# Optimization experiments

Measured on AMD Instinct MI355X. Metric: run time of the kernel, lower is better.

Reference implementation:

```python
import jax, jax.numpy as jnp
import numpy as np

EPS = 1e-5

def conv1x1(x, w, b):
    # x: [B,C,H,W], w: [O,C], b: [O]
    return jnp.einsum('bchw,oc->bohw', x, w) + b[None, :, None, None]

def bn(x, gamma, beta, mean, var):
    scale = gamma / jnp.sqrt(var + EPS)
    return x * scale[None, :, None, None] + (beta - mean * scale)[None, :, None, None]

def setup_inputs() -> dict:
    B, C, H, W = 8, 256, 64, 64
    F0, F1 = 128, 128
    key = jax.random.key(0)
    ks = jax.random.split(key, 16)
    d = {}
    d['inputs'] = jax.random.normal(ks[0], (B, C, H, W), dtype=jnp.float32)
    def make_cna(i, fout, fin):
        w = jax.random.normal(ks[i], (fout, fin), dtype=jnp.float32) / np.sqrt(fin)
        b = jnp.zeros((fout,), dtype=jnp.float32)
        g = jnp.ones((fout,), dtype=jnp.float32)
        be = jnp.zeros((fout,), dtype=jnp.float32)
        m = 0.1 * jax.random.normal(ks[i + 1], (fout,), dtype=jnp.float32)
        v = jax.random.uniform(ks[i + 2], (fout,), dtype=jnp.float32, minval=0.5, maxval=1.5)
        return w, b, g, be, m, v
    (d['theta_w'], d['theta_b'], d['theta_g'], d['theta_beta'], d['theta_m'], d['theta_v']) = make_cna(1, F0, C)
    (d['phi_w'], d['phi_b'], d['phi_g'], d['phi_beta'], d['phi_m'], d['phi_v']) = make_cna(4, F0, C)
    (d['mu_w'], d['mu_b'], d['mu_g'], d['mu_beta'], d['mu_m'], d['mu_v']) = make_cna(7, F1, C)
    d['pre_w'] = jax.random.normal(ks[10], (C, F1), dtype=jnp.float32) / np.sqrt(F1)
    d['pre_b'] = jnp.zeros((C,), dtype=jnp.float32)
    d['post_g'] = jnp.ones((C,), dtype=jnp.float32)
    d['post_beta'] = jnp.zeros((C,), dtype=jnp.float32)
    d['post_m'] = 0.1 * jax.random.normal(ks[11], (C,), dtype=jnp.float32)
    d['post_v'] = jax.random.uniform(ks[12], (C,), dtype=jnp.float32, minval=0.5, maxval=1.5)
    return d

def reference(inputs, theta_w, theta_b, theta_g, theta_beta, theta_m, theta_v,
              phi_w, phi_b, phi_g, phi_beta, phi_m, phi_v,
              mu_w, mu_b, mu_g, mu_beta, mu_m, mu_v,
              pre_w, pre_b, post_g, post_beta, post_m, post_v):
    B, C, H, W = inputs.shape
    N = H * W
    # theta/phi/mu: 1x1 conv + batchnorm (eval) + relu
    t = jax.nn.relu(bn(conv1x1(inputs, theta_w, theta_b), theta_g, theta_beta, theta_m, theta_v))
    p = jax.nn.relu(bn(conv1x1(inputs, phi_w, phi_b), phi_g, phi_beta, phi_m, phi_v))
    z = jax.nn.relu(bn(conv1x1(inputs, mu_w, mu_b), mu_g, mu_beta, mu_m, mu_v))
    tf = t.reshape(B, -1, N)   # [B,F0,N]
    pf = p.reshape(B, -1, N)   # [B,F0,N]
    zf = z.reshape(B, -1, N)   # [B,F1,N]
    # unscaled softmax(theta^T phi) mu^T, batched (original loops over B)
    attn = jax.nn.softmax(jnp.einsum('bfn,bfm->bnm', tf, pf), axis=-1)  # [B,N,N]
    u = jnp.einsum('bnm,bfm->bfn', attn, zf).reshape(B, -1, H, W)       # [B,F1,H,W]
    pre = conv1x1(u, pre_w, pre_b)                                       # [B,C,H,W]
    return jax.nn.relu(bn(pre + inputs, post_g, post_beta, post_m, post_v))
```

## Files before the change

### kernel.cpp

```cpp
#include <hip/hip_runtime.h>

typedef __attribute__((ext_vector_type(8))) _Float16 f16x8;
typedef __attribute__((ext_vector_type(4))) float f32x4;
typedef __attribute__((ext_vector_type(16))) float f32x16;
typedef __attribute__((ext_vector_type(4))) unsigned u32x4;

#define EPSV 1e-5f
#define BB 8
#define CC 256
#define NP 4096
#define FF 128
#define SPLIT 4
#define CHUNK 1024
#define NIT 16

#define GLD16(gp, lp) __builtin_amdgcn_global_load_lds( \
    (const __attribute__((address_space(1))) unsigned int*)(gp), \
    (__attribute__((address_space(3))) unsigned int*)(lp), 16, 0, 0)

static __device__ __forceinline__ unsigned short f2h(float f) {
    union { _Float16 h; unsigned short u; } v;
    v.h = (_Float16)f;
    return v.u;
}
static __device__ __forceinline__ float h2f(unsigned short u) {
    union { unsigned short u; _Float16 h; } v;
    v.u = u;
    return (float)v.h;
}

struct PrepArgs {
    const float* w[3]; const float* bias[3]; const float* g[3]; const float* be[3];
    const float* m[3]; const float* v[3];
    const float* pre_w; const float* pre_b;
    const float* post_g; const float* post_be; const float* post_m; const float* post_v;
    unsigned short* W_all; float* b_all; unsigned short* W2; float* b2; float* sres;
};

__global__ __launch_bounds__(256) void prep_kernel(PrepArgs a) {
    int idx = blockIdx.x * 256 + threadIdx.x;
    if (idx < 3 * 128 * 256) {
        int row = idx >> 8, c = idx & 255;
        int which = row >> 7, f = row & 127;
        float s = a.g[which][f] * rsqrtf(a.v[which][f] + EPSV);
        a.W_all[idx] = f2h(a.w[which][f * 256 + c] * s);
        if (c == 0)
            a.b_all[row] = s * a.bias[which][f] + a.be[which][f] - a.m[which][f] * s;
    } else {
        int i = idx - 3 * 128 * 256;
        if (i < 256 * 128) {
            int c = i >> 7, f = i & 127;
            float s = a.post_g[c] * rsqrtf(a.post_v[c] + EPSV);
            a.W2[i] = f2h(a.pre_w[i] * s);
            if (f == 0) {
                a.b2[c] = s * a.pre_b[c] + a.post_be[c] - a.post_m[c] * s;
                a.sres[c] = s;
            }
        }
    }
}

__global__ __launch_bounds__(256) void transpose_x_kernel(const float* __restrict__ x,
                                                          unsigned short* __restrict__ xT) {
    __shared__ float tile[64][65];
    int blk = blockIdx.x;
    int b  = blk >> 8;
    int c0 = ((blk >> 6) & 3) << 6;
    int n0 = (blk & 63) << 6;
    int t = threadIdx.x;
    const float* src = x + ((size_t)b * CC + c0) * NP + n0;
    #pragma unroll
    for (int i = 0; i < 16; ++i) {
        int cl = i * 4 + (t >> 6);
        tile[cl][t & 63] = src[(size_t)cl * NP + (t & 63)];
    }
    __syncthreads();
    unsigned short* dst = xT + ((size_t)b * NP + n0) * CC + c0;
    #pragma unroll
    for (int i = 0; i < 8; ++i) {
        int nl = i * 8 + (t >> 5);
        int cl = (t & 31) * 2;
        unsigned lo = f2h(tile[cl][nl]);
        unsigned hi = f2h(tile[cl + 1][nl]);
        *reinterpret_cast<unsigned*>(dst + (size_t)nl * CC + cl) = (hi << 16) | lo;
    }
}

__global__ __launch_bounds__(256) void qkv_kernel(const unsigned short* __restrict__ xT,
                                                  const unsigned short* __restrict__ W_all,
                                                  const float* __restrict__ b_all,
                                                  unsigned short* __restrict__ tq,
                                                  unsigned short* __restrict__ kp,
                                                  unsigned short* __restrict__ vz) {
    __shared__ unsigned short Alds[128 * 72];
    __shared__ unsigned short Blds[128 * 72];
    int blk = blockIdx.x;
    int b  = blk & 7;
    int r  = blk >> 3;
    int ft = r >> 5;
    int n0 = (r & 31) << 7;
    int fbase = ft << 7;
    int t = threadIdx.x, w = t >> 6, l = t & 63;
    int wr = (w >> 1) << 6, wc = (w & 1) << 6;
    const unsigned short* A  = xT + ((size_t)b * NP + n0) * CC;
    const unsigned short* Bw = W_all + (size_t)fbase * CC;

    f32x4 acc[4][4];
    #pragma unroll
    for (int i = 0; i < 4; ++i)
        #pragma unroll
        for (int j = 0; j < 4; ++j)
            acc[i][j] = f32x4{0.f, 0.f, 0.f, 0.f};

    for (int c0 = 0; c0 < 256; c0 += 64) {
        #pragma unroll
        for (int i = 0; i < 4; ++i) {
            int row = i * 32 + (t >> 3);
            int ch = (t & 7) * 8;
            *reinterpret_cast<int4*>(&Alds[row * 72 + ch]) =
                *reinterpret_cast<const int4*>(A + (size_t)row * CC + c0 + ch);
            *reinterpret_cast<int4*>(&Blds[row * 72 + ch]) =
                *reinterpret_cast<const int4*>(Bw + (size_t)row * CC + c0 + ch);
        }
        __syncthreads();
        #pragma unroll
        for (int kk = 0; kk < 2; ++kk) {
            f16x8 af[4], bfr[4];
            #pragma unroll
            for (int mi = 0; mi < 4; ++mi)
                af[mi] = *reinterpret_cast<const f16x8*>(
                    &Alds[(wr + mi * 16 + (l & 15)) * 72 + kk * 32 + (l >> 4) * 8]);
            #pragma unroll
            for (int ni = 0; ni < 4; ++ni)
                bfr[ni] = *reinterpret_cast<const f16x8*>(
                    &Blds[(wc + ni * 16 + (l & 15)) * 72 + kk * 32 + (l >> 4) * 8]);
            #pragma unroll
            for (int mi = 0; mi < 4; ++mi)
                #pragma unroll
                for (int ni = 0; ni < 4; ++ni)
                    acc[mi][ni] = __builtin_amdgcn_mfma_f32_16x16x32_f16(af[mi], bfr[ni], acc[mi][ni], 0, 0, 0);
        }
        __syncthreads();
    }

    #pragma unroll
    for (int mi = 0; mi < 4; ++mi) {
        #pragma unroll
        for (int ni = 0; ni < 4; ++ni) {
            int fl = wc + ni * 16 + (l & 15);
            float bias = b_all[fbase + fl];
            int nb = n0 + wr + mi * 16 + ((l >> 4) << 2);
            if (ft == 2) {
                unsigned pk0, pk1;
                float v0 = acc[mi][ni][0] + bias; v0 = v0 > 0.f ? v0 : 0.f;
                float v1 = acc[mi][ni][1] + bias; v1 = v1 > 0.f ? v1 : 0.f;
                float v2 = acc[mi][ni][2] + bias; v2 = v2 > 0.f ? v2 : 0.f;
                float v3 = acc[mi][ni][3] + bias; v3 = v3 > 0.f ? v3 : 0.f;
                pk0 = (unsigned)f2h(v0) | ((unsigned)f2h(v1) << 16);
                pk1 = (unsigned)f2h(v2) | ((unsigned)f2h(v3) << 16);
                uint2 uu; uu.x = pk0; uu.y = pk1;
                *reinterpret_cast<uint2*>(vz + (size_t)b * FF * NP + (size_t)fl * NP + nb) = uu;
            } else {
                unsigned short* dst = (ft == 0 ? tq : kp) + (size_t)b * NP * FF;
                #pragma unroll
                for (int rg = 0; rg < 4; ++rg) {
                    float v = acc[mi][ni][rg] + bias;
                    dst[(size_t)(nb + rg) * FF + fl] = f2h(v > 0.f ? v : 0.f);
                }
            }
        }
    }
}

__global__ __launch_bounds__(256, 2) void attn_kernel(const unsigned short* __restrict__ tq,
                                                      const unsigned short* __restrict__ kp,
                                                      const unsigned short* __restrict__ vz,
                                                      unsigned short* __restrict__ Uh,
                                                      float2* __restrict__ ml) {
    __shared__ unsigned short Kl[2][8192];
    __shared__ unsigned short Vl[2][8192];
    int blk = blockIdx.x;
    int b = blk & 7;
    int rest = blk >> 3;
    int s = rest & 3;
    int qt = rest >> 2;
    int t = threadIdx.x, w = t >> 6, l = t & 63;
    int r = l & 31, h = l >> 5, lx = l & 7;
    int n0w = qt * 128 + w * 32;
    int mbase = s * CHUNK;
    const unsigned short* Q = tq + (size_t)b * NP * FF;
    const unsigned short* K = kp + (size_t)b * NP * FF;
    const unsigned short* V = vz + (size_t)b * FF * NP;

    f16x8 qf[8];
    #pragma unroll
    for (int kf = 0; kf < 8; ++kf)
        qf[kf] = *reinterpret_cast<const f16x8*>(Q + (size_t)(n0w + r) * FF + kf * 16 + h * 8);

    f32x16 U[4];
    #pragma unroll
    for (int fb = 0; fb < 4; ++fb)
        #pragma unroll
        for (int i = 0; i < 16; ++i) U[fb][i] = 0.f;
    float mrun = -1e30f, lrun = 0.f;

    const unsigned short* kbase[4];
    const unsigned short* vbase[4];
    #pragma unroll
    for (int i = 0; i < 4; ++i) {
        int seg = w * 4 + i;
        int krow = seg * 4 + (l >> 4);
        kbase[i] = K + (size_t)(mbase + krow) * FF + 8 * ((l & 15) ^ (krow & 7));
        int frow = seg * 8 + (l >> 3);
        vbase[i] = V + (size_t)frow * NP + mbase + 8 * ((l & 7) ^ (frow & 7));
    }

    #pragma unroll
    for (int i = 0; i < 4; ++i) {
        GLD16(kbase[i], &Kl[0][(w * 4 + i) * 512]);
        GLD16(vbase[i], &Vl[0][(w * 4 + i) * 512]);
    }

    int cur = 0;
    for (int it = 0; it < NIT; ++it) {
        asm volatile("s_waitcnt vmcnt(0)" ::: "memory");
        __builtin_amdgcn_s_barrier();
        asm volatile("" ::: "memory");
        if (it + 1 < NIT) {
            #pragma unroll
            for (int i = 0; i < 4; ++i) {
                GLD16(kbase[i] + (size_t)(it + 1) * 64 * FF, &Kl[cur ^ 1][(w * 4 + i) * 512]);
                GLD16(vbase[i] + (it + 1) * 64, &Vl[cur ^ 1][(w * 4 + i) * 512]);
            }
        }
        const unsigned short* Kb = Kl[cur];
        const unsigned short* Vb = Vl[cur];

        f32x16 St0, St1;
        #pragma unroll
        for (int i = 0; i < 16; ++i) { St0[i] = 0.f; St1[i] = 0.f; }
        __builtin_amdgcn_s_setprio(1);
        #pragma unroll
        for (int kf = 0; kf < 8; ++kf) {
            f16x8 a0 = *reinterpret_cast<const f16x8*>(Kb + r * 128 + 8 * ((2 * kf + h) ^ lx));
            f16x8 a1 = *reinterpret_cast<const f16x8*>(Kb + (32 + r) * 128 + 8 * ((2 * kf + h) ^ lx));
            St0 = __builtin_amdgcn_mfma_f32_32x32x16_f16(a0, qf[kf], St0, 0, 0, 0);
            St1 = __builtin_amdgcn_mfma_f32_32x32x16_f16(a1, qf[kf], St1, 0, 0, 0);
        }
        __builtin_amdgcn_s_setprio(0);

        float pmax = St0[0];
        #pragma unroll
        for (int i = 1; i < 16; ++i) pmax = fmaxf(pmax, St0[i]);
        #pragma unroll
        for (int i = 0; i < 16; ++i) pmax = fmaxf(pmax, St1[i]);
        pmax = fmaxf(pmax, __shfl_xor(pmax, 32));
        if (__any(pmax > mrun + 8.0f)) {
            float mnew = fmaxf(mrun, pmax);
            float sc = __expf(mrun - mnew);
            mrun = mnew; lrun *= sc;
            #pragma unroll
            for (int rr = 0; rr < 16; ++rr) {
                float scb = __shfl(sc, (rr & 3) + 8 * (rr >> 2) + 4 * h);
                U[0][rr] *= scb; U[1][rr] *= scb; U[2][rr] *= scb; U[3][rr] *= scb;
            }
        }
        float lsum = 0.f;
        unsigned pka[8], pkb[8];
        #pragma unroll
        for (int rr = 0; rr < 8; ++rr) {
            float e0 = __expf(St0[2 * rr] - mrun);
            float e1 = __expf(St0[2 * rr + 1] - mrun);
            float e2 = __expf(St1[2 * rr] - mrun);
            float e3 = __expf(St1[2 * rr + 1] - mrun);
            lsum += (e0 + e1) + (e2 + e3);
            pka[rr] = __builtin_bit_cast(unsigned, __builtin_amdgcn_cvt_pkrtz(e0, e1));
            pkb[rr] = __builtin_bit_cast(unsigned, __builtin_amdgcn_cvt_pkrtz(e2, e3));
        }
        lsum += __shfl_xor(lsum, 32);
        lrun += lsum;

        __builtin_amdgcn_s_setprio(1);
        #pragma unroll
        for (int kb = 0; kb < 4; ++kb) {
            int ib = 4 * (kb & 1);
            unsigned p0 = (kb < 2) ? pka[ib + 0] : pkb[ib + 0];
            unsigned p1 = (kb < 2) ? pka[ib + 1] : pkb[ib + 1];
            unsigned p2 = (kb < 2) ? pka[ib + 2] : pkb[ib + 2];
            unsigned p3 = (kb < 2) ? pka[ib + 3] : pkb[ib + 3];
            unsigned x0 = __shfl_xor(p0, 32), x1 = __shfl_xor(p1, 32);
            unsigned y0 = __shfl_xor(p2, 32), y1 = __shfl_xor(p3, 32);
            u32x4 du;
            du[0] = h ? y0 : p0;
            du[1] = h ? y1 : p1;
            du[2] = h ? p2 : x0;
            du[3] = h ? p3 : x1;
            f16x8 af = __builtin_bit_cast(f16x8, du);
            #pragma unroll
            for (int fb = 0; fb < 4; ++fb) {
                f16x8 vf = *reinterpret_cast<const f16x8*>(
                    Vb + (fb * 32 + r) * 64 + 8 * ((2 * kb + h) ^ lx));
                U[fb] = __builtin_amdgcn_mfma_f32_32x32x16_f16(af, vf, U[fb], 0, 0, 0);
            }
        }
        __builtin_amdgcn_s_setprio(0);
        cur ^= 1;
    }

    float linv = 1.0f / lrun;
    unsigned short* up = Uh + (size_t)(s * 8 + b) * NP * FF;
    #pragma unroll
    for (int rr = 0; rr < 16; ++rr) {
        int nn = (rr & 3) + 8 * (rr >> 2) + 4 * h;
        float scb = __shfl(linv, nn);
        int n = n0w + nn;
        #pragma unroll
        for (int fb = 0; fb < 4; ++fb)
            up[(size_t)n * FF + fb * 32 + r] = f2h(U[fb][rr] * scb);
    }
    if (l < 32)
        ml[(size_t)(s * 8 + b) * NP + n0w + l] = make_float2(mrun, lrun);
}

__global__ __launch_bounds__(256) void combine_kernel(const unsigned short* __restrict__ Uh,
                                                      const float2* __restrict__ ml,
                                                      unsigned short* __restrict__ uT) {
    int row = blockIdx.x * 2 + (threadIdx.x >> 7);
    int f = threadIdx.x & 127;
    float m[SPLIT], lv[SPLIT];
    #pragma unroll
    for (int s = 0; s < SPLIT; ++s) {
        float2 v = ml[(size_t)s * (BB * NP) + row];
        m[s] = v.x; lv[s] = v.y;
    }
    float M = fmaxf(fmaxf(m[0], m[1]), fmaxf(m[2], m[3]));
    float wsum = 0.f, acc = 0.f;
    #pragma unroll
    for (int s = 0; s < SPLIT; ++s) {
        float wgt = __expf(m[s] - M) * lv[s];
        wsum += wgt;
        acc += wgt * h2f(Uh[((size_t)s * (BB * NP) + row) * FF + f]);
    }
    uT[(size_t)row * FF + f] = f2h(acc / wsum);
}

__global__ __launch_bounds__(256) void final_kernel(const unsigned short* __restrict__ uT,
                                                    const unsigned short* __restrict__ W2,
                                                    const float* __restrict__ b2,
                                                    const float* __restrict__ sres,
                                                    const float* __restrict__ x,
                                                    float* __restrict__ out) {
    __shared__ unsigned short Alds[128 * 72];
    __shared__ unsigned short Blds[128 * 72];
    int blk = blockIdx.x;
    int b  = blk & 7;
    int r  = blk >> 3;
    int ct = r & 1;
    int nt = r >> 1;
    int c0 = ct << 7, n0 = nt << 7;
    int t = threadIdx.x, w = t >> 6, l = t & 63;
    int wr = (w >> 1) << 6, wc = (w & 1) << 6;

    f32x4 acc[4][4];
    #pragma unroll
    for (int i = 0; i < 4; ++i)
        #pragma unroll
        for (int j = 0; j < 4; ++j)
            acc[i][j] = f32x4{0.f, 0.f, 0.f, 0.f};

    for (int k0 = 0; k0 < 128; k0 += 64) {
        #pragma unroll
        for (int i = 0; i < 4; ++i) {
            int row = i * 32 + (t >> 3);
            int ch = (t & 7) * 8;
            *reinterpret_cast<int4*>(&Alds[row * 72 + ch]) =
                *reinterpret_cast<const int4*>(W2 + (size_t)(c0 + row) * FF + k0 + ch);
            *reinterpret_cast<int4*>(&Blds[row * 72 + ch]) =
                *reinterpret_cast<const int4*>(uT + ((size_t)b * NP + n0 + row) * FF + k0 + ch);
        }
        __syncthreads();
        #pragma unroll
        for (int kk = 0; kk < 2; ++kk) {
            f16x8 af[4], bfr[4];
            #pragma unroll
            for (int mi = 0; mi < 4; ++mi)
                af[mi] = *reinterpret_cast<const f16x8*>(
                    &Alds[(wr + mi * 16 + (l & 15)) * 72 + kk * 32 + (l >> 4) * 8]);
            #pragma unroll
            for (int ni = 0; ni < 4; ++ni)
                bfr[ni] = *reinterpret_cast<const f16x8*>(
                    &Blds[(wc + ni * 16 + (l & 15)) * 72 + kk * 32 + (l >> 4) * 8]);
            #pragma unroll
            for (int mi = 0; mi < 4; ++mi)
                #pragma unroll
                for (int ni = 0; ni < 4; ++ni)
                    acc[mi][ni] = __builtin_amdgcn_mfma_f32_16x16x32_f16(af[mi], bfr[ni], acc[mi][ni], 0, 0, 0);
        }
        __syncthreads();
    }

    const float* xb = x + (size_t)b * CC * NP;
    float* ob = out + (size_t)b * CC * NP;
    #pragma unroll
    for (int mi = 0; mi < 4; ++mi)
        #pragma unroll
        for (int ni = 0; ni < 4; ++ni) {
            int n = n0 + wc + ni * 16 + (l & 15);
            int cb = c0 + wr + mi * 16 + ((l >> 4) << 2);
            #pragma unroll
            for (int rg = 0; rg < 4; ++rg) {
                int c = cb + rg;
                float v = acc[mi][ni][rg] + b2[c] + sres[c] * xb[(size_t)c * NP + n];
                ob[(size_t)c * NP + n] = v > 0.f ? v : 0.f;
            }
        }
}

extern "C" void kernel_launch(void* const* d_in, const int* in_sizes, int n_in,
                              void* d_out, int out_size, void* d_ws, size_t ws_size,
                              hipStream_t stream) {
    const float* x = (const float*)d_in[0];
    char* ws = (char*)d_ws;
    unsigned short* W_all = (unsigned short*)(ws);
    float*          b_all = (float*)(ws + 196608);
    unsigned short* W2    = (unsigned short*)(ws + 198144);
    float*          b2    = (float*)(ws + 263680);
    float*          sres  = (float*)(ws + 264704);
    unsigned short* xT    = (unsigned short*)(ws + 265728);
    unsigned short* tq    = (unsigned short*)(ws + 17042944);
    unsigned short* kp    = (unsigned short*)(ws + 25431552);
    unsigned short* vz    = (unsigned short*)(ws + 33820160);
    unsigned short* uT    = (unsigned short*)(ws + 42208768);
    unsigned short* Uh    = (unsigned short*)(ws + 50597376);
    float2*         ml    = (float2*)(ws + 84151808);

    PrepArgs pa;
    pa.w[0]  = (const float*)d_in[1];  pa.bias[0] = (const float*)d_in[2];
    pa.g[0]  = (const float*)d_in[3];  pa.be[0]   = (const float*)d_in[4];
    pa.m[0]  = (const float*)d_in[5];  pa.v[0]    = (const float*)d_in[6];
    pa.w[1]  = (const float*)d_in[7];  pa.bias[1] = (const float*)d_in[8];
    pa.g[1]  = (const float*)d_in[9];  pa.be[1]   = (const float*)d_in[10];
    pa.m[1]  = (const float*)d_in[11]; pa.v[1]    = (const float*)d_in[12];
    pa.w[2]  = (const float*)d_in[13]; pa.bias[2] = (const float*)d_in[14];
    pa.g[2]  = (const float*)d_in[15]; pa.be[2]   = (const float*)d_in[16];
    pa.m[2]  = (const float*)d_in[17]; pa.v[2]    = (const float*)d_in[18];
    pa.pre_w = (const float*)d_in[19]; pa.pre_b   = (const float*)d_in[20];
    pa.post_g = (const float*)d_in[21]; pa.post_be = (const float*)d_in[22];
    pa.post_m = (const float*)d_in[23]; pa.post_v  = (const float*)d_in[24];
    pa.W_all = W_all; pa.b_all = b_all; pa.W2 = W2; pa.b2 = b2; pa.sres = sres;

    prep_kernel<<<dim3(512), dim3(256), 0, stream>>>(pa);
    transpose_x_kernel<<<dim3(2048), dim3(256), 0, stream>>>(x, xT);
    qkv_kernel<<<dim3(768), dim3(256), 0, stream>>>(xT, W_all, b_all, tq, kp, vz);
    attn_kernel<<<dim3(1024), dim3(256), 0, stream>>>(tq, kp, vz, Uh, ml);
    combine_kernel<<<dim3(16384), dim3(256), 0, stream>>>(Uh, ml, uT);
    final_kernel<<<dim3(512), dim3(256), 0, stream>>>(uT, W2, b2, sres, x, (float*)d_out);
}
```

Baseline: 266.2 us.

## Store Q/K/V in MFMA-fragment order and load K fragments directly to registers

The qkv kernel now writes Q, K and V in a pre-swizzled layout that matches the 32x32x16 MFMA operand fragments, so the attention kernel can read them with contiguous per-lane 16-byte loads. K is no longer staged through LDS but is prefetched straight into registers, and the key tile shrinks from 64 to 32 per iteration (NIT 32), which halves LDS use and raises launch bounds occupancy to 3 blocks per CU. Cross-half exchanges use permlane32_swap instead of shuffles. The risks are more loop iterations with more barriers, scattered 2-byte global stores in qkv, and higher register pressure from holding the K fragments.

```diff
diff --git a/kernel.cpp b/kernel.cpp
--- a/kernel.cpp
+++ b/kernel.cpp
@@ -4,6 +4,7 @@
 typedef __attribute__((ext_vector_type(4))) float f32x4;
 typedef __attribute__((ext_vector_type(16))) float f32x16;
 typedef __attribute__((ext_vector_type(4))) unsigned u32x4;
+typedef __attribute__((ext_vector_type(2))) unsigned u32x2;
 
 #define EPSV 1e-5f
 #define BB 8
@@ -12,7 +13,7 @@
 #define FF 128
 #define SPLIT 4
 #define CHUNK 1024
-#define NIT 16
+#define NIT 32
 
 #define GLD16(gp, lp) __builtin_amdgcn_global_load_lds( \
     (const __attribute__((address_space(1))) unsigned int*)(gp), \
@@ -28,6 +29,12 @@
     v.u = u;
     return (float)v.h;
 }
+static __device__ __forceinline__ void plswap(unsigned& a, unsigned& b) {
+    u32x2 r = __builtin_amdgcn_permlane32_swap(a, b, false, false);
+    a = r[0]; b = r[1];
+}
+static __device__ __forceinline__ unsigned fbits(float f) { return __builtin_bit_cast(unsigned, f); }
+static __device__ __forceinline__ float bitsf(unsigned u) { return __builtin_bit_cast(float, u); }
 
 struct PrepArgs {
     const float* w[3]; const float* bias[3]; const float* g[3]; const float* be[3];
@@ -89,9 +96,9 @@
 __global__ __launch_bounds__(256) void qkv_kernel(const unsigned short* __restrict__ xT,
                                                   const unsigned short* __restrict__ W_all,
                                                   const float* __restrict__ b_all,
-                                                  unsigned short* __restrict__ tq,
-                                                  unsigned short* __restrict__ kp,
-                                                  unsigned short* __restrict__ vz) {
+                                                  unsigned short* __restrict__ qT,
+                                                  unsigned short* __restrict__ kT,
+                                                  unsigned short* __restrict__ vT) {
     __shared__ unsigned short Alds[128 * 72];
     __shared__ unsigned short Blds[128 * 72];
     int blk = blockIdx.x;
@@ -150,52 +157,58 @@
             int fl = wc + ni * 16 + (l & 15);
             float bias = b_all[fbase + fl];
             int nb = n0 + wr + mi * 16 + ((l >> 4) << 2);
+            float v0 = acc[mi][ni][0] + bias; v0 = v0 > 0.f ? v0 : 0.f;
+            float v1 = acc[mi][ni][1] + bias; v1 = v1 > 0.f ? v1 : 0.f;
+            float v2 = acc[mi][ni][2] + bias; v2 = v2 > 0.f ? v2 : 0.f;
+            float v3 = acc[mi][ni][3] + bias; v3 = v3 > 0.f ? v3 : 0.f;
             if (ft == 2) {
-                unsigned pk0, pk1;
-                float v0 = acc[mi][ni][0] + bias; v0 = v0 > 0.f ? v0 : 0.f;
-                float v1 = acc[mi][ni][1] + bias; v1 = v1 > 0.f ? v1 : 0.f;
-                float v2 = acc[mi][ni][2] + bias; v2 = v2 > 0.f ? v2 : 0.f;
-                float v3 = acc[mi][ni][3] + bias; v3 = v3 > 0.f ? v3 : 0.f;
-                pk0 = (unsigned)f2h(v0) | ((unsigned)f2h(v1) << 16);
-                pk1 = (unsigned)f2h(v2) | ((unsigned)f2h(v3) << 16);
-                uint2 uu; uu.x = pk0; uu.y = pk1;
-                *reinterpret_cast<uint2*>(vz + (size_t)b * FF * NP + (size_t)fl * NP + nb) = uu;
+                int mtile = nb >> 5, kb = (nb >> 4) & 1, hh = (nb >> 3) & 1, j = nb & 7;
+                int fb = fl >> 5, rcol = fl & 31;
+                unsigned short* dst = vT + (size_t)b * NP * FF +
+                    (size_t)mtile * 4096 + (size_t)(fb * 2 + kb) * 512 + (hh * 32 + rcol) * 8 + j;
+                uint2 uu;
+                uu.x = (unsigned)f2h(v0) | ((unsigned)f2h(v1) << 16);
+                uu.y = (unsigned)f2h(v2) | ((unsigned)f2h(v3) << 16);
+                *reinterpret_cast<uint2*>(dst) = uu;
             } else {
-                unsigned short* dst = (ft == 0 ? tq : kp) + (size_t)b * NP * FF;
-                #pragma unroll
-                for (int rg = 0; rg < 4; ++rg) {
-                    float v = acc[mi][ni][rg] + bias;
-                    dst[(size_t)(nb + rg) * FF + fl] = f2h(v > 0.f ? v : 0.f);
-                }
+                unsigned short* dst = (ft == 0 ? qT : kT) + (size_t)b * NP * FF;
+                int kf = fl >> 4, hh = (fl >> 3) & 1, j = fl & 7;
+                unsigned short h0 = f2h(v0), h1 = f2h(v1), h2 = f2h(v2), h3 = f2h(v3);
+                dst[(size_t)((nb + 0) >> 5) * 4096 + kf * 512 + (hh * 32 + ((nb + 0) & 31)) * 8 + j] = h0;
+                dst[(size_t)((nb + 1) >> 5) * 4096 + kf * 512 + (hh * 32 + ((nb + 1) & 31)) * 8 + j] = h1;
+                dst[(size_t)((nb + 2) >> 5) * 4096 + kf * 512 + (hh * 32 + ((nb + 2) & 31)) * 8 + j] = h2;
+                dst[(size_t)((nb + 3) >> 5) * 4096 + kf * 512 + (hh * 32 + ((nb + 3) & 31)) * 8 + j] = h3;
             }
         }
     }
 }
 
-__global__ __launch_bounds__(256, 2) void attn_kernel(const unsigned short* __restrict__ tq,
-                                                      const unsigned short* __restrict__ kp,
-                                                      const unsigned short* __restrict__ vz,
+__global__ __launch_bounds__(256, 3) void attn_kernel(const unsigned short* __restrict__ qT,
+                                                      const unsigned short* __restrict__ kT,
+                                                      const unsigned short* __restrict__ vT,
                                                       unsigned short* __restrict__ Uh,
                                                       float2* __restrict__ ml) {
-    __shared__ unsigned short Kl[2][8192];
-    __shared__ unsigned short Vl[2][8192];
+    __shared__ unsigned short Vl[2][4096];
     int blk = blockIdx.x;
     int b = blk & 7;
     int rest = blk >> 3;
     int s = rest & 3;
     int qt = rest >> 2;
     int t = threadIdx.x, w = t >> 6, l = t & 63;
-    int r = l & 31, h = l >> 5, lx = l & 7;
+    int r = l & 31, h = l >> 5;
     int n0w = qt * 128 + w * 32;
-    int mbase = s * CHUNK;
-    const unsigned short* Q = tq + (size_t)b * NP * FF;
-    const unsigned short* K = kp + (size_t)b * NP * FF;
-    const unsigned short* V = vz + (size_t)b * FF * NP;
-
-    f16x8 qf[8];
-    #pragma unroll
-    for (int kf = 0; kf < 8; ++kf)
-        qf[kf] = *reinterpret_cast<const f16x8*>(Q + (size_t)(n0w + r) * FF + kf * 16 + h * 8);
+    const unsigned short* Qb = qT + (size_t)b * NP * FF + (size_t)(qt * 4 + w) * 4096;
+    const unsigned short* Kb = kT + (size_t)b * NP * FF + (size_t)(s * 32) * 4096;
+    const unsigned short* Vb = vT + (size_t)b * NP * FF + (size_t)(s * 32) * 4096;
+
+    f16x8 qf[8], kg[8];
+    #pragma unroll
+    for (int kf = 0; kf < 8; ++kf) {
+        qf[kf] = *reinterpret_cast<const f16x8*>(Qb + kf * 512 + l * 8);
+        kg[kf] = *reinterpret_cast<const f16x8*>(Kb + kf * 512 + l * 8);
+    }
+    GLD16(Vb + w * 512 + l * 8, &Vl[0][w * 512]);
+    GLD16(Vb + 2048 + w * 512 + l * 8, &Vl[0][2048 + w * 512]);
 
     f32x16 U[4];
     #pragma unroll
@@ -203,23 +216,6 @@
         #pragma unroll
         for (int i = 0; i < 16; ++i) U[fb][i] = 0.f;
     float mrun = -1e30f, lrun = 0.f;
-
-    const unsigned short* kbase[4];
-    const unsigned short* vbase[4];
-    #pragma unroll
-    for (int i = 0; i < 4; ++i) {
-        int seg = w * 4 + i;
-        int krow = seg * 4 + (l >> 4);
-        kbase[i] = K + (size_t)(mbase + krow) * FF + 8 * ((l & 15) ^ (krow & 7));
-        int frow = seg * 8 + (l >> 3);
-        vbase[i] = V + (size_t)frow * NP + mbase + 8 * ((l & 7) ^ (frow & 7));
-    }
-
-    #pragma unroll
-    for (int i = 0; i < 4; ++i) {
-        GLD16(kbase[i], &Kl[0][(w * 4 + i) * 512]);
-        GLD16(vbase[i], &Vl[0][(w * 4 + i) * 512]);
-    }
 
     int cur = 0;
     for (int it = 0; it < NIT; ++it) {
@@ -227,34 +223,33 @@
         __builtin_amdgcn_s_barrier();
         asm volatile("" ::: "memory");
         if (it + 1 < NIT) {
-            #pragma unroll
-            for (int i = 0; i < 4; ++i) {
-                GLD16(kbase[i] + (size_t)(it + 1) * 64 * FF, &Kl[cur ^ 1][(w * 4 + i) * 512]);
-                GLD16(vbase[i] + (it + 1) * 64, &Vl[cur ^ 1][(w * 4 + i) * 512]);
-            }
-        }
-        const unsigned short* Kb = Kl[cur];
-        const unsigned short* Vb = Vl[cur];
-
-        f32x16 St0, St1;
-        #pragma unroll
-        for (int i = 0; i < 16; ++i) { St0[i] = 0.f; St1[i] = 0.f; }
+            const unsigned short* vn = Vb + (size_t)(it + 1) * 4096;
+            GLD16(vn + w * 512 + l * 8, &Vl[cur ^ 1][w * 512]);
+            GLD16(vn + 2048 + w * 512 + l * 8, &Vl[cur ^ 1][2048 + w * 512]);
+        }
+
+        f32x16 St;
+        #pragma unroll
+        for (int i = 0; i < 16; ++i) St[i] = 0.f;
         __builtin_amdgcn_s_setprio(1);
         #pragma unroll
-        for (int kf = 0; kf < 8; ++kf) {
-            f16x8 a0 = *reinterpret_cast<const f16x8*>(Kb + r * 128 + 8 * ((2 * kf + h) ^ lx));
-            f16x8 a1 = *reinterpret_cast<const f16x8*>(Kb + (32 + r) * 128 + 8 * ((2 * kf + h) ^ lx));
-            St0 = __builtin_amdgcn_mfma_f32_32x32x16_f16(a0, qf[kf], St0, 0, 0, 0);
-            St1 = __builtin_amdgcn_mfma_f32_32x32x16_f16(a1, qf[kf], St1, 0, 0, 0);
-        }
+        for (int kf = 0; kf < 8; ++kf)
+            St = __builtin_amdgcn_mfma_f32_32x32x16_f16(kg[kf], qf[kf], St, 0, 0, 0);
         __builtin_amdgcn_s_setprio(0);
 
-        float pmax = St0[0];
-        #pragma unroll
-        for (int i = 1; i < 16; ++i) pmax = fmaxf(pmax, St0[i]);
-        #pragma unroll
-        for (int i = 0; i < 16; ++i) pmax = fmaxf(pmax, St1[i]);
-        pmax = fmaxf(pmax, __shfl_xor(pmax, 32));
+        if (it + 1 < NIT) {
+            const unsigned short* kn = Kb + (size_t)(it + 1) * 4096;
+            #pragma unroll
+            for (int kf = 0; kf < 8; ++kf)
+                kg[kf] = *reinterpret_cast<const f16x8*>(kn + kf * 512 + l * 8);
+        }
+
+        float pm0 = fmaxf(fmaxf(St[0], St[1]), fmaxf(St[2], St[3]));
+        float pm1 = fmaxf(fmaxf(St[4], St[5]), fmaxf(St[6], St[7]));
+        float pm2 = fmaxf(fmaxf(St[8], St[9]), fmaxf(St[10], St[11]));
+        float pm3 = fmaxf(fmaxf(St[12], St[13]), fmaxf(St[14], St[15]));
+        float pmax = fmaxf(fmaxf(pm0, pm1), fmaxf(pm2, pm3));
+        { unsigned pa = fbits(pmax), pb = pa; plswap(pa, pb); pmax = fmaxf(bitsf(pa), bitsf(pb)); }
         if (__any(pmax > mrun + 8.0f)) {
             float mnew = fmaxf(mrun, pmax);
             float sc = __expf(mrun - mnew);
@@ -266,40 +261,30 @@
             }
         }
         float lsum = 0.f;
-        unsigned pka[8], pkb[8];
-        #pragma unroll
-        for (int rr = 0; rr < 8; ++rr) {
-            float e0 = __expf(St0[2 * rr] - mrun);
-            float e1 = __expf(St0[2 * rr + 1] - mrun);
-            float e2 = __expf(St1[2 * rr] - mrun);
-            float e3 = __expf(St1[2 * rr + 1] - mrun);
-            lsum += (e0 + e1) + (e2 + e3);
-            pka[rr] = __builtin_bit_cast(unsigned, __builtin_amdgcn_cvt_pkrtz(e0, e1));
-            pkb[rr] = __builtin_bit_cast(unsigned, __builtin_amdgcn_cvt_pkrtz(e2, e3));
-        }
-        lsum += __shfl_xor(lsum, 32);
+        unsigned pk[8];
+        #pragma unroll
+        for (int i = 0; i < 8; ++i) {
+            float e0 = __expf(St[2 * i] - mrun);
+            float e1 = __expf(St[2 * i + 1] - mrun);
+            lsum += e0 + e1;
+            pk[i] = __builtin_bit_cast(unsigned, __builtin_amdgcn_cvt_pkrtz(e0, e1));
+        }
+        { unsigned la = fbits(lsum), lb = la; plswap(la, lb); lsum = bitsf(la) + bitsf(lb); }
         lrun += lsum;
 
+        const unsigned short* Vc = &Vl[cur][0];
         __builtin_amdgcn_s_setprio(1);
         #pragma unroll
-        for (int kb = 0; kb < 4; ++kb) {
-            int ib = 4 * (kb & 1);
-            unsigned p0 = (kb < 2) ? pka[ib + 0] : pkb[ib + 0];
-            unsigned p1 = (kb < 2) ? pka[ib + 1] : pkb[ib + 1];
-            unsigned p2 = (kb < 2) ? pka[ib + 2] : pkb[ib + 2];
-            unsigned p3 = (kb < 2) ? pka[ib + 3] : pkb[ib + 3];
-            unsigned x0 = __shfl_xor(p0, 32), x1 = __shfl_xor(p1, 32);
-            unsigned y0 = __shfl_xor(p2, 32), y1 = __shfl_xor(p3, 32);
-            u32x4 du;
-            du[0] = h ? y0 : p0;
-            du[1] = h ? y1 : p1;
-            du[2] = h ? p2 : x0;
-            du[3] = h ? p3 : x1;
+        for (int kb = 0; kb < 2; ++kb) {
+            unsigned a0 = pk[kb * 4 + 0], b0 = pk[kb * 4 + 2];
+            unsigned a1 = pk[kb * 4 + 1], b1 = pk[kb * 4 + 3];
+            plswap(a0, b0);
+            plswap(a1, b1);
+            u32x4 du; du[0] = a0; du[1] = a1; du[2] = b0; du[3] = b1;
             f16x8 af = __builtin_bit_cast(f16x8, du);
             #pragma unroll
             for (int fb = 0; fb < 4; ++fb) {
-                f16x8 vf = *reinterpret_cast<const f16x8*>(
-                    Vb + (fb * 32 + r) * 64 + 8 * ((2 * kb + h) ^ lx));
+                f16x8 vf = *reinterpret_cast<const f16x8*>(Vc + (fb * 2 + kb) * 512 + l * 8);
                 U[fb] = __builtin_amdgcn_mfma_f32_32x32x16_f16(af, vf, U[fb], 0, 0, 0);
             }
         }
@@ -427,9 +412,9 @@
     float*          b2    = (float*)(ws + 263680);
     float*          sres  = (float*)(ws + 264704);
     unsigned short* xT    = (unsigned short*)(ws + 265728);
-    unsigned short* tq    = (unsigned short*)(ws + 17042944);
-    unsigned short* kp    = (unsigned short*)(ws + 25431552);
-    unsigned short* vz    = (unsigned short*)(ws + 33820160);
+    unsigned short* qT    = (unsigned short*)(ws + 17042944);
+    unsigned short* kT    = (unsigned short*)(ws + 25431552);
+    unsigned short* vT    = (unsigned short*)(ws + 33820160);
     unsigned short* uT    = (unsigned short*)(ws + 42208768);
     unsigned short* Uh    = (unsigned short*)(ws + 50597376);
     float2*         ml    = (float2*)(ws + 84151808);
@@ -451,8 +436,8 @@
 
     prep_kernel<<<dim3(512), dim3(256), 0, stream>>>(pa);
     transpose_x_kernel<<<dim3(2048), dim3(256), 0, stream>>>(x, xT);
-    qkv_kernel<<<dim3(768), dim3(256), 0, stream>>>(xT, W_all, b_all, tq, kp, vz);
-    attn_kernel<<<dim3(1024), dim3(256), 0, stream>>>(tq, kp, vz, Uh, ml);
+    qkv_kernel<<<dim3(768), dim3(256), 0, stream>>>(xT, W_all, b_all, qT, kT, vT);
+    attn_kernel<<<dim3(1024), dim3(256), 0, stream>>>(qT, kT, vT, Uh, ml);
     combine_kernel<<<dim3(16384), dim3(256), 0, stream>>>(Uh, ml, uT);
     final_kernel<<<dim3(512), dim3(256), 0, stream>>>(uT, W2, b2, sres, x, (float*)d_out);
 }
```

Measured after the change: 271.7 us. +2.1%, slower.
